# Kernel optimization log

Hardware: AMD Instinct MI355X
Metric: run time of the kernel (lower is better)

Reference implementation:

```python
import jax, jax.numpy as jnp
import numpy as np

N_NODES = 100000
D = 128            # node feature dim == hidden_units[0]
N_EDGES = 640000
BN_EPS = 1e-3      # keras BatchNormalization default epsilon


def setup_inputs() -> dict:
    key = jax.random.key(0)
    ks = jax.random.split(key, 12)
    node_repr = jax.random.normal(ks[0], (N_NODES, D), dtype=jnp.float32)
    edges = jax.random.randint(ks[1], (2, N_EDGES), 0, N_NODES, dtype=jnp.int64)
    # ffn_prepare: BN(D) -> Dense(D, gelu)   (dropout inactive at inference)
    bn1_gamma = jax.random.normal(ks[2], (D,), dtype=jnp.float32) * 0.1 + 1.0
    bn1_beta = jax.random.normal(ks[3], (D,), dtype=jnp.float32) * 0.1
    bn1_mean = jax.random.normal(ks[4], (D,), dtype=jnp.float32) * 0.1
    bn1_var = jax.random.uniform(ks[5], (D,), dtype=jnp.float32) + 0.5
    W1 = jax.random.normal(ks[6], (D, D), dtype=jnp.float32) / np.sqrt(D)
    b1 = jnp.zeros((D,), dtype=jnp.float32)
    # update_fn: BN(2D) -> Dense(D, gelu)
    bn2_gamma = jax.random.normal(ks[7], (2 * D,), dtype=jnp.float32) * 0.1 + 1.0
    bn2_beta = jax.random.normal(ks[8], (2 * D,), dtype=jnp.float32) * 0.1
    bn2_mean = jax.random.normal(ks[9], (2 * D,), dtype=jnp.float32) * 0.1
    bn2_var = jax.random.uniform(ks[10], (2 * D,), dtype=jnp.float32) + 0.5
    W2 = jax.random.normal(ks[11], (2 * D, D), dtype=jnp.float32) / np.sqrt(2 * D)
    b2 = jnp.zeros((D,), dtype=jnp.float32)
    return dict(node_repr=node_repr, edges=edges,
                bn1_gamma=bn1_gamma, bn1_beta=bn1_beta, bn1_mean=bn1_mean, bn1_var=bn1_var,
                W1=W1, b1=b1,
                bn2_gamma=bn2_gamma, bn2_beta=bn2_beta, bn2_mean=bn2_mean, bn2_var=bn2_var,
                W2=W2, b2=b2)


def _bn(x, gamma, beta, mean, var):
    # inference-mode batch norm
    return (x - mean) * jax.lax.rsqrt(var + BN_EPS) * gamma + beta


def reference(node_repr, edges, bn1_gamma, bn1_beta, bn1_mean, bn1_var, W1, b1,
              bn2_gamma, bn2_beta, bn2_mean, bn2_var, W2, b2):
    num_nodes = node_repr.shape[0]
    node_indices, neighbour_indices = edges[0], edges[1]
    # gather neighbour features: [E, D]
    neigh = node_repr[neighbour_indices]
    # prepare FFN (BN -> dropout(identity at eval) -> Dense + exact gelu)
    msg = jax.nn.gelu(_bn(neigh, bn1_gamma, bn1_beta, bn1_mean, bn1_var) @ W1 + b1,
                      approximate=False)
    # unsorted_segment_mean: sum / count, empty segments -> 0 (TF semantics)
    sums = jax.ops.segment_sum(msg, node_indices, num_segments=num_nodes)
    cnt = jax.ops.segment_sum(jnp.ones((edges.shape[1],), msg.dtype), node_indices,
                              num_segments=num_nodes)
    agg = sums / jnp.maximum(cnt, 1.0)[:, None]
    # update FFN on concat [node_repr, agg]: [N, 2D] -> [N, D]
    h = jnp.concatenate([node_repr, agg], axis=1)
    out = jax.nn.gelu(_bn(h, bn2_gamma, bn2_beta, bn2_mean, bn2_var) @ W2 + b2,
                      approximate=False)
    return out
```

## Files before the change

### kernel.cpp

```cpp
#include <hip/hip_runtime.h>

#define NN 100000
#define DD 128
#define EE 640000
#define BN_EPS 1e-3f
#define NBLK 391
#define NTILE 6250
#define EPB 1637
#define FFN1_BLKS 1563
#define FFN2_BLKS 768

typedef __bf16 bf16x8 __attribute__((ext_vector_type(8)));
typedef float f32x4 __attribute__((ext_vector_type(4)));

#define W1F_OFF 0u
#define W2F_OFF 32768u
#define B1F_OFF 98304u
#define B2F_OFF 98816u
#define T_OFF   99328u
#define OFFS_OFF 26099328u
#define ELIST_OFF 26899328u
#define CNTG_OFF ELIST_OFF
#define BOFS_OFF (ELIST_OFF + 611524u)
#define BSUM_OFF 29459328u
#define AGG_OFF 29464576u
#define XB_OFF  55064576u

__device__ __forceinline__ float gelu_fast(float x) {
    float x3 = x * x * x;
    float z2 = 1.5957691216057308f * x + 0.07135481627002407f * x3;
    return x / (1.0f + __expf(-z2));
}

__global__ __launch_bounds__(256) void prep_kernel(
    const float* __restrict__ g1, const float* __restrict__ be1,
    const float* __restrict__ m1, const float* __restrict__ v1,
    const float* __restrict__ W1, const float* __restrict__ b1,
    const float* __restrict__ g2, const float* __restrict__ be2,
    const float* __restrict__ m2, const float* __restrict__ v2,
    const float* __restrict__ W2, const float* __restrict__ b2,
    const int* __restrict__ edges,
    __bf16* __restrict__ W1f, __bf16* __restrict__ W2f,
    float* __restrict__ b1f, float* __restrict__ b2f,
    int* __restrict__ cntg)
{
    const int blk = blockIdx.x;
    const int t = threadIdx.x;
    if (blk < 64) {
        const int w = (blk * 256 + t) >> 6;
        const int lane = t & 63;
        if (w < 128) {
            float acc = 0.f;
            for (int k = lane; k < 128; k += 64) {
                float s = g1[k] * rsqrtf(v1[k] + BN_EPS);
                float sh = be1[k] - m1[k] * s;
                acc += sh * W1[k * 128 + w];
            }
#pragma unroll
            for (int off = 32; off > 0; off >>= 1) acc += __shfl_down(acc, off);
            if (lane == 0) b1f[w] = acc + b1[w];
        } else {
            const int n = w - 128;
            float acc = 0.f;
            for (int k = lane; k < 256; k += 64) {
                float s = g2[k] * rsqrtf(v2[k] + BN_EPS);
                float sh = be2[k] - m2[k] * s;
                acc += sh * W2[k * 128 + n];
            }
#pragma unroll
            for (int off = 32; off > 0; off >>= 1) acc += __shfl_down(acc, off);
            if (lane == 0) b2f[n] = acc + b2[n];
        }
    } else if (blk < 256) {
        int tid = (blk - 64) * 256 + t;
        if (tid < 16384) {
            int idx = tid;
            int i = idx & 7, l = (idx >> 3) & 63, nt = (idx >> 9) & 7, kt = idx >> 12;
            int k = kt * 32 + (l >> 4) * 8 + i;
            int n = nt * 16 + (l & 15);
            float s = g1[k] * rsqrtf(v1[k] + BN_EPS);
            W1f[idx] = (__bf16)(s * W1[k * 128 + n]);
        } else {
            int idx = tid - 16384;
            int i = idx & 7, l = (idx >> 3) & 63, nt = (idx >> 9) & 7, kt = idx >> 12;
            int n = nt * 16 + (l & 15);
            int row;
            if (kt < 4) {
                row = kt * 32 + (l >> 4) * 8 + i;
            } else {
                int q = (kt - 4) * 32 + (l >> 4) * 8 + i;
                row = 128 + ((q & 7) * 16 + (q >> 3));
            }
            float s = g2[row] * rsqrtf(v2[row] + BN_EPS);
            W2f[idx] = (__bf16)(s * W2[row * 128 + n]);
        }
    } else {
        __shared__ int cnt[NBLK];
        const int k = blk - 256;
        for (int b = t; b < NBLK; b += 256) cnt[b] = 0;
        __syncthreads();
        const int e0 = k * EPB, e1 = min(e0 + EPB, EE);
        for (int e = e0 + t; e < e1; e += 256)
            atomicAdd(&cnt[edges[e] >> 8], 1);
        __syncthreads();
        for (int b = t; b < NBLK; b += 256) cntg[k * NBLK + b] = cnt[b];
    }
}

__global__ __launch_bounds__(256) void sortb_kernel(const int* __restrict__ cntg,
                                                    int* __restrict__ bofs,
                                                    int* __restrict__ bsum)
{
    const int b = blockIdx.x, t = threadIdx.x;
    __shared__ int sp[256];
    int ia = 2 * t, ib = 2 * t + 1;
    int va = (ia < NBLK) ? cntg[ia * NBLK + b] : 0;
    int vb = (ib < NBLK) ? cntg[ib * NBLK + b] : 0;
    sp[t] = va + vb;
    __syncthreads();
    for (int off = 1; off < 256; off <<= 1) {
        int tmp = (t >= off) ? sp[t - off] : 0;
        __syncthreads();
        sp[t] += tmp;
        __syncthreads();
    }
    int pexcl = sp[t] - (va + vb);
    if (ia < NBLK) bofs[b * NBLK + ia] = pexcl;
    if (ib < NBLK) bofs[b * NBLK + ib] = pexcl + va;
    if (t == 255) bsum[b] = sp[255];
}

__global__ __launch_bounds__(256) void sortc_kernel(const int* __restrict__ edges,
                                                    const int* __restrict__ bsum,
                                                    const int* __restrict__ bofs,
                                                    int* __restrict__ pairbuf)
{
    __shared__ int sp[256];
    __shared__ int cur[NBLK];
    const int k = blockIdx.x, t = threadIdx.x;
    int ia = 2 * t, ib = 2 * t + 1;
    int va = (ia < NBLK) ? bsum[ia] : 0;
    int vb = (ib < NBLK) ? bsum[ib] : 0;
    sp[t] = va + vb;
    __syncthreads();
    for (int off = 1; off < 256; off <<= 1) {
        int tmp = (t >= off) ? sp[t - off] : 0;
        __syncthreads();
        sp[t] += tmp;
        __syncthreads();
    }
    int pexcl = sp[t] - (va + vb);
    if (ia < NBLK) cur[ia] = pexcl + bofs[ia * NBLK + k];
    if (ib < NBLK) cur[ib] = pexcl + va + bofs[ib * NBLK + k];
    __syncthreads();
    const int e0 = k * EPB, e1 = min(e0 + EPB, EE);
    for (int e = e0 + t; e < e1; e += 256) {
        int dst = edges[e];
        int src = edges[EE + e];
        int pos = atomicAdd(&cur[dst >> 8], 1);
        pairbuf[pos] = (src << 8) | (dst & 255);
    }
}

__global__ __launch_bounds__(256) void p2_ffn1_kernel(
    const int* __restrict__ bsum, const int* __restrict__ pairbuf,
    int* __restrict__ elist, int* __restrict__ offs,
    const float* __restrict__ X, const __bf16* __restrict__ W1f,
    const float* __restrict__ b1f, __bf16* __restrict__ T,
    __bf16* __restrict__ Xb)
{
    __shared__ int sArr[256];
    __shared__ int cur[256];
    __shared__ int red[4];
    const int t = threadIdx.x;
    if (blockIdx.x < NBLK) {
        const int b = blockIdx.x;
        int part = 0;
        for (int i = t; i < b; i += 256) part += bsum[i];
#pragma unroll
        for (int off = 32; off > 0; off >>= 1) part += __shfl_down(part, off);
        if ((t & 63) == 0) red[t >> 6] = part;
        cur[t] = 0;
        __syncthreads();
        const int start = red[0] + red[1] + red[2] + red[3];
        const int end = start + bsum[b];
        for (int e = start + t; e < end; e += 256)
            atomicAdd(&cur[pairbuf[e] & 255], 1);
        __syncthreads();
        int v = cur[t];
        sArr[t] = v;
        __syncthreads();
        for (int off = 1; off < 256; off <<= 1) {
            int tmp = (t >= off) ? sArr[t - off] : 0;
            __syncthreads();
            sArr[t] += tmp;
            __syncthreads();
        }
        int ex = sArr[t] - v + start;
        const int node = b * 256 + t;
        if (node <= NN) offs[node] = ex;
        __syncthreads();
        cur[t] = ex;
        __syncthreads();
        for (int e = start + t; e < end; e += 256) {
            int item = pairbuf[e];
            int pos = atomicAdd(&cur[item & 255], 1);
            elist[pos] = item >> 8;
        }
        return;
    }

    const int wave = t >> 6;
    const int lane = t & 63;
    const int tile = (blockIdx.x - NBLK) * 4 + wave;
    if (tile >= NTILE) return;
    const int c = lane & 15, kh = lane >> 4;

    const size_t rowb = (size_t)(tile * 16 + c) * DD;
    const float* xr = X + rowb + kh * 8;

    f32x4 r0[4], r1[4];
#pragma unroll
    for (int q = 0; q < 4; ++q) {
        r0[q] = *(const f32x4*)(xr + q * 32);
        r1[q] = *(const f32x4*)(xr + q * 32 + 4);
    }
    bf16x8 bp[8], bq[8];
#pragma unroll
    for (int nt = 0; nt < 8; ++nt)
        bp[nt] = *(const bf16x8*)(W1f + ((size_t)(nt * 64 + lane)) * 8);

    bf16x8 af[4];
#pragma unroll
    for (int kt = 0; kt < 4; ++kt) {
        bf16x8 fa;
#pragma unroll
        for (int i = 0; i < 4; ++i) { fa[i] = (__bf16)r0[kt][i]; fa[4 + i] = (__bf16)r1[kt][i]; }
        af[kt] = fa;
        *(bf16x8*)(Xb + rowb + kt * 32 + kh * 8) = fa;
    }

    f32x4 acc[8] = {};
#pragma unroll
    for (int kt = 0; kt < 4; ++kt) {
        if (kt + 1 < 4) {
#pragma unroll
            for (int nt = 0; nt < 8; ++nt) {
                bf16x8 v = *(const bf16x8*)(W1f + ((size_t)(((kt + 1) * 8 + nt) * 64 + lane)) * 8);
                if (kt & 1) bp[nt] = v; else bq[nt] = v;
            }
        }
#pragma unroll
        for (int nt = 0; nt < 8; ++nt) {
            bf16x8 curb = (kt & 1) ? bq[nt] : bp[nt];
            acc[nt] = __builtin_amdgcn_mfma_f32_16x16x32_bf16(af[kt], curb, acc[nt], 0, 0, 0);
        }
    }

    float bias[8];
#pragma unroll
    for (int nt = 0; nt < 8; ++nt) bias[nt] = b1f[nt * 16 + c];

#pragma unroll
    for (int r = 0; r < 4; ++r) {
        int row = tile * 16 + kh * 4 + r;
        bf16x8 o;
#pragma unroll
        for (int nt = 0; nt < 8; ++nt)
            o[nt] = (__bf16)gelu_fast(acc[nt][r] + bias[nt]);
        *(bf16x8*)(T + (size_t)row * DD + c * 8) = o;
    }
}

__global__ __launch_bounds__(256) void agg_kernel(
    const __bf16* __restrict__ T, const int* __restrict__ offs,
    const int* __restrict__ elist, __bf16* __restrict__ Agg)
{
    int t = blockIdx.x * 256 + threadIdx.x;
    int node = t >> 4, j = t & 15;
    if (node >= NN) return;
    const int lane = threadIdx.x & 63;
    const int gbase = lane & 48;
    const int beg = offs[node];
    const int end = offs[node + 1];
    const int d = end - beg;
    float acc[8] = {};
    for (int eb = beg; eb < end; eb += 16) {
        int me = eb + (lane & 15);
        int sv = (me < end) ? elist[me] : 0;
        int cnt = min(end - eb, 16);
        int i = 0;
        for (; i + 3 < cnt; i += 4) {
            int s0 = __shfl(sv, gbase + i);
            int s1 = __shfl(sv, gbase + i + 1);
            int s2 = __shfl(sv, gbase + i + 2);
            int s3 = __shfl(sv, gbase + i + 3);
            bf16x8 v0 = *(const bf16x8*)(T + (size_t)s0 * DD + j * 8);
            bf16x8 v1 = *(const bf16x8*)(T + (size_t)s1 * DD + j * 8);
            bf16x8 v2 = *(const bf16x8*)(T + (size_t)s2 * DD + j * 8);
            bf16x8 v3 = *(const bf16x8*)(T + (size_t)s3 * DD + j * 8);
#pragma unroll
            for (int q = 0; q < 8; ++q)
                acc[q] += ((float)v0[q] + (float)v1[q]) + ((float)v2[q] + (float)v3[q]);
        }
        for (; i < cnt; ++i) {
            int s0 = __shfl(sv, gbase + i);
            bf16x8 v0 = *(const bf16x8*)(T + (size_t)s0 * DD + j * 8);
#pragma unroll
            for (int q = 0; q < 8; ++q) acc[q] += (float)v0[q];
        }
    }
    const float inv = 1.0f / fmaxf((float)d, 1.0f);
    bf16x8 o;
#pragma unroll
    for (int q = 0; q < 8; ++q) o[q] = (__bf16)(acc[q] * inv);
    *(bf16x8*)(Agg + (size_t)node * DD + j * 8) = o;
}

#define FFN2_LOAD(TT, XA, GA)                                              \
    {                                                                      \
        const size_t rb = (size_t)((TT) * 16 + c) * DD + kh * 8;           \
        _Pragma("unroll")                                                  \
        for (int q = 0; q < 4; ++q) {                                      \
            XA[q] = *(const bf16x8*)(Xb + rb + q * 32);                    \
            GA[q] = *(const bf16x8*)(Agg + rb + q * 32);                   \
        }                                                                  \
    }

#define FFN2_COMP(TT, XA, GA)                                              \
    {                                                                      \
        f32x4 acc0 = {}, acc1 = {};                                        \
        _Pragma("unroll")                                                  \
        for (int kt = 0; kt < 4; ++kt) {                                   \
            acc0 = __builtin_amdgcn_mfma_f32_16x16x32_bf16(XA[kt], Bf[kt][0], acc0, 0, 0, 0); \
            acc1 = __builtin_amdgcn_mfma_f32_16x16x32_bf16(XA[kt], Bf[kt][1], acc1, 0, 0, 0); \
        }                                                                  \
        _Pragma("unroll")                                                  \
        for (int kt = 0; kt < 4; ++kt) {                                   \
            acc0 = __builtin_amdgcn_mfma_f32_16x16x32_bf16(GA[kt], Bf[4 + kt][0], acc0, 0, 0, 0); \
            acc1 = __builtin_amdgcn_mfma_f32_16x16x32_bf16(GA[kt], Bf[4 + kt][1], acc1, 0, 0, 0); \
        }                                                                  \
        _Pragma("unroll")                                                  \
        for (int r = 0; r < 4; ++r) {                                      \
            int row = (TT) * 16 + kh * 4 + r;                              \
            out[(size_t)row * DD + (w * 2) * 16 + c] = gelu_fast(acc0[r] + bias0); \
            out[(size_t)row * DD + (w * 2 + 1) * 16 + c] = gelu_fast(acc1[r] + bias1); \
        }                                                                  \
    }

__global__ __launch_bounds__(256) void ffn2_kernel(
    const __bf16* __restrict__ Xb, const __bf16* __restrict__ Agg,
    const __bf16* __restrict__ W2f, const float* __restrict__ b2f,
    float* __restrict__ out)
{
    const int w = threadIdx.x >> 6;
    const int lane = threadIdx.x & 63;
    const int c = lane & 15, kh = lane >> 4;
    const int G = gridDim.x;

    bf16x8 Bf[8][2];
#pragma unroll
    for (int kt = 0; kt < 8; ++kt) {
        Bf[kt][0] = *(const bf16x8*)(W2f + ((size_t)((kt * 8 + w * 2) * 64 + lane)) * 8);
        Bf[kt][1] = *(const bf16x8*)(W2f + ((size_t)((kt * 8 + w * 2 + 1) * 64 + lane)) * 8);
    }
    const float bias0 = b2f[(w * 2) * 16 + c];
    const float bias1 = b2f[(w * 2 + 1) * 16 + c];

    int tile = blockIdx.x;
    if (tile >= NTILE) return;
    bf16x8 xa[4], ga[4], xb2[4], gb[4];
    FFN2_LOAD(tile, xa, ga);
    while (true) {
        int t2 = tile + G;
        if (t2 < NTILE) FFN2_LOAD(t2, xb2, gb);
        FFN2_COMP(tile, xa, ga);
        if (t2 >= NTILE) break;
        int t3 = t2 + G;
        if (t3 < NTILE) FFN2_LOAD(t3, xa, ga);
        FFN2_COMP(t2, xb2, gb);
        if (t3 >= NTILE) break;
        tile = t3;
    }
}

extern "C" void kernel_launch(void* const* d_in, const int* in_sizes, int n_in,
                              void* d_out, int out_size, void* d_ws, size_t ws_size,
                              hipStream_t stream) {
    const float* node_repr = (const float*)d_in[0];
    const int*   edges     = (const int*)d_in[1];
    const float* g1 = (const float*)d_in[2];
    const float* be1 = (const float*)d_in[3];
    const float* m1 = (const float*)d_in[4];
    const float* v1 = (const float*)d_in[5];
    const float* W1 = (const float*)d_in[6];
    const float* b1 = (const float*)d_in[7];
    const float* g2 = (const float*)d_in[8];
    const float* be2 = (const float*)d_in[9];
    const float* m2 = (const float*)d_in[10];
    const float* v2 = (const float*)d_in[11];
    const float* W2 = (const float*)d_in[12];
    const float* b2 = (const float*)d_in[13];

    char* ws = (char*)d_ws;
    __bf16* W1f = (__bf16*)(ws + W1F_OFF);
    __bf16* W2f = (__bf16*)(ws + W2F_OFF);
    float* b1f = (float*)(ws + B1F_OFF);
    float* b2f = (float*)(ws + B2F_OFF);
    __bf16* T  = (__bf16*)(ws + T_OFF);
    int* offs  = (int*)(ws + OFFS_OFF);
    int* elist = (int*)(ws + ELIST_OFF);
    int* cntg  = (int*)(ws + CNTG_OFF);
    int* bofs  = (int*)(ws + BOFS_OFF);
    int* bsum  = (int*)(ws + BSUM_OFF);
    __bf16* Agg = (__bf16*)(ws + AGG_OFF);
    int* pairbuf = (int*)(ws + AGG_OFF);
    __bf16* Xb = (__bf16*)(ws + XB_OFF);
    float* out = (float*)d_out;

    hipLaunchKernelGGL(prep_kernel, dim3(256 + NBLK), dim3(256), 0, stream,
                       g1, be1, m1, v1, W1, b1, g2, be2, m2, v2, W2, b2,
                       edges, W1f, W2f, b1f, b2f, cntg);

    hipLaunchKernelGGL(sortb_kernel, dim3(NBLK), dim3(256), 0, stream, cntg, bofs, bsum);

    hipLaunchKernelGGL(sortc_kernel, dim3(NBLK), dim3(256), 0, stream,
                       edges, bsum, bofs, pairbuf);

    hipLaunchKernelGGL(p2_ffn1_kernel, dim3(NBLK + FFN1_BLKS), dim3(256), 0, stream,
                       bsum, pairbuf, elist, offs, node_repr, W1f, b1f, T, Xb);

    hipLaunchKernelGGL(agg_kernel, dim3((NN * 16 + 255) / 256), dim3(256), 0, stream,
                       T, offs, elist, Agg);

    hipLaunchKernelGGL(ffn2_kernel, dim3(FFN2_BLKS), dim3(256), 0, stream,
                       Xb, Agg, W2f, b2f, out);
}
```

Measured before the change: 103.2 us.

## Make FFN1 persistent with register-resident weights and double-buffered X loads

The FFN1 phase now runs as a persistent grid of 768 blocks instead of one block per group of 4 tiles. Within each block the four waves split the 128 output columns, each wave computing 32. Every wave keeps its slice of W1 in registers for the whole kernel and prefetches the next tile's X rows while computing the current one. The column order of T changes to match the new wave split, and the W2 agg-row permutation is updated to follow it. The goal is to remove the repeated weight loads and hide X load latency. The cost is that every wave reads the full X tile, so each block reads X four times from cache.

Result: slower. 117.3 us (+13.7%).

```diff
diff --git a/kernel.cpp b/kernel.cpp
--- a/kernel.cpp
+++ b/kernel.cpp
@@ -7,10 +7,11 @@
 #define NBLK 391
 #define NTILE 6250
 #define EPB 1637
-#define FFN1_BLKS 1563
+#define FFN1_BLKS 768
 #define FFN2_BLKS 768
 
 typedef __bf16 bf16x8 __attribute__((ext_vector_type(8)));
+typedef __bf16 bf16x2 __attribute__((ext_vector_type(2)));
 typedef float f32x4 __attribute__((ext_vector_type(4)));
 
 #define W1F_OFF 0u
@@ -89,7 +90,7 @@
                 row = kt * 32 + (l >> 4) * 8 + i;
             } else {
                 int q = (kt - 4) * 32 + (l >> 4) * 8 + i;
-                row = 128 + ((q & 7) * 16 + (q >> 3));
+                row = 128 + ((2 * (q >> 5) + (q & 1)) * 16 + ((q >> 1) & 15));
             }
             float s = g2[row] * rsqrtf(v2[row] + BN_EPS);
             W2f[idx] = (__bf16)(s * W2[row * 128 + n]);
@@ -162,6 +163,50 @@
     }
 }
 
+#define FFN1_XLD(TT, RA, RB)                                               \
+    {                                                                      \
+        const float* xr = X + (size_t)((TT) * 16 + c) * DD + kh * 8;       \
+        _Pragma("unroll")                                                  \
+        for (int q = 0; q < 4; ++q) {                                      \
+            RA[q] = *(const f32x4*)(xr + q * 32);                          \
+            RB[q] = *(const f32x4*)(xr + q * 32 + 4);                      \
+        }                                                                  \
+    }
+
+#define FFN1_CMP(TT, RA, RB)                                               \
+    {                                                                      \
+        bf16x8 af[4];                                                      \
+        _Pragma("unroll")                                                  \
+        for (int kt = 0; kt < 4; ++kt) {                                   \
+            bf16x8 fa;                                                     \
+            _Pragma("unroll")                                              \
+            for (int i = 0; i < 4; ++i) {                                  \
+                fa[i] = (__bf16)RA[kt][i]; fa[4 + i] = (__bf16)RB[kt][i];  \
+            }                                                              \
+            af[kt] = fa;                                                   \
+        }                                                                  \
+        if (w == 0) {                                                      \
+            const size_t rowb = (size_t)((TT) * 16 + c) * DD;              \
+            _Pragma("unroll")                                              \
+            for (int kt = 0; kt < 4; ++kt)                                 \
+                *(bf16x8*)(Xb + rowb + kt * 32 + kh * 8) = af[kt];         \
+        }                                                                  \
+        f32x4 a0 = {}, a1 = {};                                            \
+        _Pragma("unroll")                                                  \
+        for (int kt = 0; kt < 4; ++kt) {                                   \
+            a0 = __builtin_amdgcn_mfma_f32_16x16x32_bf16(af[kt], Bf1[kt][0], a0, 0, 0, 0); \
+            a1 = __builtin_amdgcn_mfma_f32_16x16x32_bf16(af[kt], Bf1[kt][1], a1, 0, 0, 0); \
+        }                                                                  \
+        _Pragma("unroll")                                                  \
+        for (int r = 0; r < 4; ++r) {                                      \
+            int rowp = (TT) * 16 + kh * 4 + r;                             \
+            bf16x2 pk;                                                     \
+            pk[0] = (__bf16)gelu_fast(a0[r] + bias0);                      \
+            pk[1] = (__bf16)gelu_fast(a1[r] + bias1);                      \
+            *(bf16x2*)(T + (size_t)rowp * DD + w * 32 + c * 2) = pk;       \
+        }                                                                  \
+    }
+
 __global__ __launch_bounds__(256) void p2_ffn1_kernel(
     const int* __restrict__ bsum, const int* __restrict__ pairbuf,
     int* __restrict__ elist, int* __restrict__ offs,
@@ -210,65 +255,32 @@
         return;
     }
 
-    const int wave = t >> 6;
+    const int w = t >> 6;
     const int lane = t & 63;
-    const int tile = (blockIdx.x - NBLK) * 4 + wave;
-    if (tile >= NTILE) return;
     const int c = lane & 15, kh = lane >> 4;
 
-    const size_t rowb = (size_t)(tile * 16 + c) * DD;
-    const float* xr = X + rowb + kh * 8;
-
-    f32x4 r0[4], r1[4];
-#pragma unroll
-    for (int q = 0; q < 4; ++q) {
-        r0[q] = *(const f32x4*)(xr + q * 32);
-        r1[q] = *(const f32x4*)(xr + q * 32 + 4);
-    }
-    bf16x8 bp[8], bq[8];
-#pragma unroll
-    for (int nt = 0; nt < 8; ++nt)
-        bp[nt] = *(const bf16x8*)(W1f + ((size_t)(nt * 64 + lane)) * 8);
-
-    bf16x8 af[4];
+    bf16x8 Bf1[4][2];
 #pragma unroll
     for (int kt = 0; kt < 4; ++kt) {
-        bf16x8 fa;
-#pragma unroll
-        for (int i = 0; i < 4; ++i) { fa[i] = (__bf16)r0[kt][i]; fa[4 + i] = (__bf16)r1[kt][i]; }
-        af[kt] = fa;
-        *(bf16x8*)(Xb + rowb + kt * 32 + kh * 8) = fa;
-    }
-
-    f32x4 acc[8] = {};
-#pragma unroll
-    for (int kt = 0; kt < 4; ++kt) {
-        if (kt + 1 < 4) {
-#pragma unroll
-            for (int nt = 0; nt < 8; ++nt) {
-                bf16x8 v = *(const bf16x8*)(W1f + ((size_t)(((kt + 1) * 8 + nt) * 64 + lane)) * 8);
-                if (kt & 1) bp[nt] = v; else bq[nt] = v;
-            }
-        }
-#pragma unroll
-        for (int nt = 0; nt < 8; ++nt) {
-            bf16x8 curb = (kt & 1) ? bq[nt] : bp[nt];
-            acc[nt] = __builtin_amdgcn_mfma_f32_16x16x32_bf16(af[kt], curb, acc[nt], 0, 0, 0);
-        }
-    }
-
-    float bias[8];
-#pragma unroll
-    for (int nt = 0; nt < 8; ++nt) bias[nt] = b1f[nt * 16 + c];
-
-#pragma unroll
-    for (int r = 0; r < 4; ++r) {
-        int row = tile * 16 + kh * 4 + r;
-        bf16x8 o;
-#pragma unroll
-        for (int nt = 0; nt < 8; ++nt)
-            o[nt] = (__bf16)gelu_fast(acc[nt][r] + bias[nt]);
-        *(bf16x8*)(T + (size_t)row * DD + c * 8) = o;
+        Bf1[kt][0] = *(const bf16x8*)(W1f + ((size_t)((kt * 8 + w * 2) * 64 + lane)) * 8);
+        Bf1[kt][1] = *(const bf16x8*)(W1f + ((size_t)((kt * 8 + w * 2 + 1) * 64 + lane)) * 8);
+    }
+    const float bias0 = b1f[(w * 2) * 16 + c];
+    const float bias1 = b1f[(w * 2 + 1) * 16 + c];
+
+    int tile = blockIdx.x - NBLK;
+    f32x4 ra[4], rb[4], sa[4], sb[4];
+    FFN1_XLD(tile, ra, rb);
+    while (true) {
+        int t2 = tile + FFN1_BLKS;
+        if (t2 < NTILE) FFN1_XLD(t2, sa, sb);
+        FFN1_CMP(tile, ra, rb);
+        if (t2 >= NTILE) break;
+        int t3 = t2 + FFN1_BLKS;
+        if (t3 < NTILE) FFN1_XLD(t3, ra, rb);
+        FFN1_CMP(t2, sa, sb);
+        if (t3 >= NTILE) break;
+        tile = t3;
     }
 }
 
```
